# Kernel tuning notes

Measured on AMD Instinct MI355X. Metric: run time of the kernel, lower is better.

Reference implementation:

```python
import jax, jax.numpy as jnp
import numpy as np

MODE_STATIC = 0
MODE_APPEARANCE_CHANGE = 2
MODE_BLINK = 3
MODE_AFFINE = 4


def _affine_warp(src, theta):
    """F.affine_grid + F.grid_sample(bilinear, zeros, align_corners=False).

    src:   [N, C, H, W]
    theta: [N, 2, 3]
    """
    N, C, H, W = src.shape
    dt = src.dtype
    # affine_grid base coords (align_corners=False): centers of pixels in [-1, 1]
    xs = (jnp.arange(W, dtype=dt) * 2 + 1) / W - 1  # [W]
    ys = (jnp.arange(H, dtype=dt) * 2 + 1) / H - 1  # [H]
    gx = (theta[:, 0, 0][:, None, None] * xs[None, None, :]
          + theta[:, 0, 1][:, None, None] * ys[None, :, None]
          + theta[:, 0, 2][:, None, None])  # [N, H, W]
    gy = (theta[:, 1, 0][:, None, None] * xs[None, None, :]
          + theta[:, 1, 1][:, None, None] * ys[None, :, None]
          + theta[:, 1, 2][:, None, None])  # [N, H, W]
    # unnormalize (align_corners=False)
    ix = ((gx + 1) * W - 1) / 2
    iy = ((gy + 1) * H - 1) / 2
    x0 = jnp.floor(ix)
    y0 = jnp.floor(iy)
    wx1 = ix - x0
    wy1 = iy - y0
    wx0 = 1 - wx1
    wy0 = 1 - wy1
    x0i = x0.astype(jnp.int32)
    y0i = y0.astype(jnp.int32)

    src_flat = src.reshape(N, C, H * W)

    def gather(xi, yi):
        valid = (xi >= 0) & (xi < W) & (yi >= 0) & (yi < H)  # zeros padding
        xi_c = jnp.clip(xi, 0, W - 1)
        yi_c = jnp.clip(yi, 0, H - 1)
        idx = (yi_c * W + xi_c).reshape(N, 1, H * W)
        v = jnp.take_along_axis(src_flat, idx, axis=2).reshape(N, C, H, W)
        return v * valid.astype(dt)[:, None]

    out = (gather(x0i, y0i) * (wx0 * wy0)[:, None]
           + gather(x0i + 1, y0i) * (wx1 * wy0)[:, None]
           + gather(x0i, y0i + 1) * (wx0 * wy1)[:, None]
           + gather(x0i + 1, y0i + 1) * (wx1 * wy1)[:, None])
    return out


def setup_inputs() -> dict:
    key = jax.random.key(0)
    ks = jax.random.split(key, 7)
    B, NI, C, H, W = 4, 16, 3, 256, 256
    g0 = jax.random.normal(ks[0], (B, NI, C, H, W), dtype=jnp.float32)
    m0 = jax.random.uniform(ks[1], (B, NI, 1, H, W), dtype=jnp.float32)
    mode_logits = jax.random.normal(ks[2], (B, NI, 5), dtype=jnp.float32)
    # near-identity affine transforms (realistic small motions)
    ident = jnp.array([1.0, 0.0, 0.0, 0.0, 1.0, 0.0], dtype=jnp.float32)
    transform_params = ident + 0.1 * jax.random.normal(ks[3], (B, NI, 6), dtype=jnp.float32)
    alpha = jax.random.uniform(ks[4], (B, NI, 1), dtype=jnp.float32)
    instance_valid = (jax.random.uniform(ks[5], (B, NI)) > 0.2).astype(jnp.float32)
    i_bg = jax.random.normal(ks[6], (B, C, H, W), dtype=jnp.float32)
    return {"g0": g0, "m0": m0, "mode_logits": mode_logits,
            "transform_params": transform_params, "alpha": alpha,
            "instance_valid": instance_valid, "i_bg": i_bg}


def reference(g0, m0, mode_logits, transform_params, alpha, instance_valid, i_bg):
    B, NI, C, H, W = g0.shape
    theta = transform_params.reshape(-1, 2, 3)  # [B*NI, 2, 3]
    warped_overlay = _affine_warp(g0.reshape(B * NI, C, H, W), theta).reshape(B, NI, C, H, W)
    warped_mask = _affine_warp(m0.reshape(B * NI, 1, H, W), theta).reshape(B, NI, 1, H, W)

    mode_ids = jnp.argmax(mode_logits, axis=-1)  # [B, NI]
    static_like = ((mode_ids == MODE_STATIC) | (mode_ids == MODE_APPEARANCE_CHANGE)
                   | (mode_ids == MODE_AFFINE)).astype(g0.dtype)[:, :, None, None, None]
    blink = (mode_ids == MODE_BLINK).astype(g0.dtype)[:, :, None, None, None]
    alpha_map = alpha[:, :, :, None, None]  # [B, NI, 1, 1, 1]
    valid = instance_valid[:, :, None, None, None]

    g_mid_per_instance = (static_like * warped_overlay + blink * warped_overlay * alpha_map) * valid
    m_mid_per_instance = (static_like * warped_mask + blink * warped_mask * alpha_map) * valid
    g_mid = g_mid_per_instance.sum(axis=1)
    m_mid = jnp.clip(m_mid_per_instance.sum(axis=1), 0.0, 1.0)
    i_base = i_bg + g_mid
    return (g_mid_per_instance, m_mid_per_instance, g_mid, m_mid, i_base)
```

## Files before the change

kernel.cpp:

```cpp
#include <hip/hip_runtime.h>

#define BB 4
#define NI 16
#define CC 3
#define HH 256
#define WW 256
#define HWSZ (HH * WW)

__device__ __forceinline__ float inst_params(
    const float* __restrict__ ml, const float* __restrict__ tp,
    const float* __restrict__ al, const float* __restrict__ iv,
    int id, float th[6]) {
    float best = ml[id * 5];
    int bid = 0;
#pragma unroll
    for (int k = 1; k < 5; ++k) {
        float v = ml[id * 5 + k];
        if (v > best) { best = v; bid = k; }
    }
    float coef = (bid == 0 || bid == 2 || bid == 4) ? 1.0f
               : (bid == 3 ? al[id] : 0.0f);
    coef *= iv[id];
#pragma unroll
    for (int k = 0; k < 6; ++k) th[k] = tp[id * 6 + k];
    return coef;
}

struct Samp {
    int o00, o10, o01, o11;
    float w00, w10, w01, w11;
};

__device__ __forceinline__ Samp make_samp(const float th[6], int p) {
    const int h = p >> 8, w = p & (WW - 1);
    const float xs = (2 * w + 1) * (1.0f / WW) - 1.0f;
    const float ys = (2 * h + 1) * (1.0f / HH) - 1.0f;
    const float gx = th[0] * xs + th[1] * ys + th[2];
    const float gy = th[3] * xs + th[4] * ys + th[5];
    const float ix = gx * (0.5f * WW) + (0.5f * WW - 0.5f);
    const float iy = gy * (0.5f * HH) + (0.5f * HH - 0.5f);
    const float x0f = floorf(ix), y0f = floorf(iy);
    const float wx1 = ix - x0f, wy1 = iy - y0f;
    const float wx0 = 1.0f - wx1, wy0 = 1.0f - wy1;
    const int x0 = (int)x0f, y0 = (int)y0f;
    const int x1 = x0 + 1, y1 = y0 + 1;
    const float wx0v = ((unsigned)x0 < (unsigned)WW) ? wx0 : 0.0f;
    const float wx1v = ((unsigned)x1 < (unsigned)WW) ? wx1 : 0.0f;
    const float wy0v = ((unsigned)y0 < (unsigned)HH) ? wy0 : 0.0f;
    const float wy1v = ((unsigned)y1 < (unsigned)HH) ? wy1 : 0.0f;
    const int x0c = min(max(x0, 0), WW - 1), x1c = min(max(x1, 0), WW - 1);
    const int y0c = min(max(y0, 0), HH - 1), y1c = min(max(y1, 0), HH - 1);
    Samp s;
    s.o00 = y0c * WW + x0c; s.o10 = y0c * WW + x1c;
    s.o01 = y1c * WW + x0c; s.o11 = y1c * WW + x1c;
    s.w00 = wx0v * wy0v; s.w10 = wx1v * wy0v;
    s.w01 = wx0v * wy1v; s.w11 = wx1v * wy1v;
    return s;
}

__device__ __forceinline__ float bilerp(const float* __restrict__ src, const Samp& s) {
    return s.w00 * src[s.o00] + s.w10 * src[s.o10]
         + s.w01 * src[s.o01] + s.w11 * src[s.o11];
}

__global__ __launch_bounds__(256) void warp_inst(
    const float* __restrict__ g0,
    const float* __restrict__ m0,
    const float* __restrict__ ml,
    const float* __restrict__ tp,
    const float* __restrict__ al,
    const float* __restrict__ iv,
    float* __restrict__ out_gpi,
    float* __restrict__ out_mpi) {
    const int id = blockIdx.y;
    const int p0 = blockIdx.x * 512 + threadIdx.x;

    float th[6];
    const float coef = inst_params(ml, tp, al, iv, id, th);

    float* gp = out_gpi + (size_t)id * CC * HWSZ + p0;
    float* mp = out_mpi + (size_t)id * HWSZ + p0;

    if (coef == 0.0f) {
        gp[0] = 0.0f;            gp[WW] = 0.0f;
        gp[HWSZ] = 0.0f;         gp[HWSZ + WW] = 0.0f;
        gp[2 * HWSZ] = 0.0f;     gp[2 * HWSZ + WW] = 0.0f;
        mp[0] = 0.0f;            mp[WW] = 0.0f;
        return;
    }

    const Samp sa = make_samp(th, p0);
    const Samp sb = make_samp(th, p0 + WW);

    const float* gsrc = g0 + (size_t)id * CC * HWSZ;
    const float* msrc = m0 + (size_t)id * HWSZ;

    const float v0a = coef * bilerp(gsrc, sa);
    const float v0b = coef * bilerp(gsrc, sb);
    const float v1a = coef * bilerp(gsrc + HWSZ, sa);
    const float v1b = coef * bilerp(gsrc + HWSZ, sb);
    const float v2a = coef * bilerp(gsrc + 2 * HWSZ, sa);
    const float v2b = coef * bilerp(gsrc + 2 * HWSZ, sb);
    const float vma = coef * bilerp(msrc, sa);
    const float vmb = coef * bilerp(msrc, sb);

    gp[0] = v0a;            gp[WW] = v0b;
    gp[HWSZ] = v1a;         gp[HWSZ + WW] = v1b;
    gp[2 * HWSZ] = v2a;     gp[2 * HWSZ + WW] = v2b;
    mp[0] = vma;            mp[WW] = vmb;
}

__global__ __launch_bounds__(128) void combine_k(
    const float* __restrict__ gpi,
    const float* __restrict__ mpi,
    const float* __restrict__ i_bg,
    float* __restrict__ out_gmid,
    float* __restrict__ out_mmid,
    float* __restrict__ out_ibase) {
    const int b = blockIdx.y;
    const int pix = (blockIdx.x * 128 + threadIdx.x) * 4;

    float4 s0 = make_float4(0.f, 0.f, 0.f, 0.f);
    float4 s1 = s0, s2 = s0, sm = s0;
#pragma unroll
    for (int ii = 0; ii < NI; ++ii) {
        const float* gb = gpi + (size_t)(b * NI + ii) * CC * HWSZ + pix;
        const float4 a0 = *(const float4*)(gb);
        const float4 a1 = *(const float4*)(gb + HWSZ);
        const float4 a2 = *(const float4*)(gb + 2 * HWSZ);
        const float4 am = *(const float4*)(mpi + (size_t)(b * NI + ii) * HWSZ + pix);
        s0.x += a0.x; s0.y += a0.y; s0.z += a0.z; s0.w += a0.w;
        s1.x += a1.x; s1.y += a1.y; s1.z += a1.z; s1.w += a1.w;
        s2.x += a2.x; s2.y += a2.y; s2.z += a2.z; s2.w += a2.w;
        sm.x += am.x; sm.y += am.y; sm.z += am.z; sm.w += am.w;
    }
    const size_t ob = (size_t)b * CC * HWSZ + pix;
    const float4 bg0 = *(const float4*)(i_bg + ob);
    const float4 bg1 = *(const float4*)(i_bg + ob + HWSZ);
    const float4 bg2 = *(const float4*)(i_bg + ob + 2 * HWSZ);

    *(float4*)(out_gmid + ob)            = s0;
    *(float4*)(out_gmid + ob + HWSZ)     = s1;
    *(float4*)(out_gmid + ob + 2 * HWSZ) = s2;
    *(float4*)(out_ibase + ob) =
        make_float4(s0.x + bg0.x, s0.y + bg0.y, s0.z + bg0.z, s0.w + bg0.w);
    *(float4*)(out_ibase + ob + HWSZ) =
        make_float4(s1.x + bg1.x, s1.y + bg1.y, s1.z + bg1.z, s1.w + bg1.w);
    *(float4*)(out_ibase + ob + 2 * HWSZ) =
        make_float4(s2.x + bg2.x, s2.y + bg2.y, s2.z + bg2.z, s2.w + bg2.w);
    *(float4*)(out_mmid + (size_t)b * HWSZ + pix) =
        make_float4(fminf(fmaxf(sm.x, 0.f), 1.f), fminf(fmaxf(sm.y, 0.f), 1.f),
                    fminf(fmaxf(sm.z, 0.f), 1.f), fminf(fmaxf(sm.w, 0.f), 1.f));
}

extern "C" void kernel_launch(void* const* d_in, const int* in_sizes, int n_in,
                              void* d_out, int out_size, void* d_ws, size_t ws_size,
                              hipStream_t stream) {
    const float* g0          = (const float*)d_in[0];
    const float* m0          = (const float*)d_in[1];
    const float* mode_logits = (const float*)d_in[2];
    const float* tp          = (const float*)d_in[3];
    const float* alpha       = (const float*)d_in[4];
    const float* iv          = (const float*)d_in[5];
    const float* i_bg        = (const float*)d_in[6];

    float* out       = (float*)d_out;
    float* out_gpi   = out;
    float* out_mpi   = out_gpi  + (size_t)BB * NI * CC * HWSZ;
    float* out_gmid  = out_mpi  + (size_t)BB * NI * HWSZ;
    float* out_mmid  = out_gmid + (size_t)BB * CC * HWSZ;
    float* out_ibase = out_mmid + (size_t)BB * HWSZ;

    dim3 grid1(HWSZ / 512, BB * NI);
    warp_inst<<<grid1, 256, 0, stream>>>(g0, m0, mode_logits, tp, alpha, iv,
                                         out_gpi, out_mpi);

    dim3 grid2(HWSZ / 4 / 128, BB);
    combine_k<<<grid2, 128, 0, stream>>>(out_gpi, out_mpi, i_bg,
                                         out_gmid, out_mmid, out_ibase);
}
```

Baseline: 155.2 us.

## Fuse per-instance warp and instance reduction into a single kernel

Merges the warp kernel and the combine kernel so each thread warps all 16 instances for one pixel, writes per-instance outputs with nontemporal stores, and accumulates the sums in registers. This removes the re-read of the full per-instance intermediate arrays and one kernel launch. In exchange, each thread processes instances serially, which lowers per-thread memory-level parallelism, and the float4 vector accesses become scalar.

```diff
diff --git a/kernel.cpp b/kernel.cpp
--- a/kernel.cpp
+++ b/kernel.cpp
@@ -63,94 +63,58 @@
          + s.w01 * src[s.o01] + s.w11 * src[s.o11];
 }
 
-__global__ __launch_bounds__(256) void warp_inst(
+__global__ __launch_bounds__(512) void fused_k(
     const float* __restrict__ g0,
     const float* __restrict__ m0,
     const float* __restrict__ ml,
     const float* __restrict__ tp,
     const float* __restrict__ al,
     const float* __restrict__ iv,
+    const float* __restrict__ i_bg,
     float* __restrict__ out_gpi,
-    float* __restrict__ out_mpi) {
-    const int id = blockIdx.y;
-    const int p0 = blockIdx.x * 512 + threadIdx.x;
-
-    float th[6];
-    const float coef = inst_params(ml, tp, al, iv, id, th);
-
-    float* gp = out_gpi + (size_t)id * CC * HWSZ + p0;
-    float* mp = out_mpi + (size_t)id * HWSZ + p0;
-
-    if (coef == 0.0f) {
-        gp[0] = 0.0f;            gp[WW] = 0.0f;
-        gp[HWSZ] = 0.0f;         gp[HWSZ + WW] = 0.0f;
-        gp[2 * HWSZ] = 0.0f;     gp[2 * HWSZ + WW] = 0.0f;
-        mp[0] = 0.0f;            mp[WW] = 0.0f;
-        return;
-    }
-
-    const Samp sa = make_samp(th, p0);
-    const Samp sb = make_samp(th, p0 + WW);
-
-    const float* gsrc = g0 + (size_t)id * CC * HWSZ;
-    const float* msrc = m0 + (size_t)id * HWSZ;
-
-    const float v0a = coef * bilerp(gsrc, sa);
-    const float v0b = coef * bilerp(gsrc, sb);
-    const float v1a = coef * bilerp(gsrc + HWSZ, sa);
-    const float v1b = coef * bilerp(gsrc + HWSZ, sb);
-    const float v2a = coef * bilerp(gsrc + 2 * HWSZ, sa);
-    const float v2b = coef * bilerp(gsrc + 2 * HWSZ, sb);
-    const float vma = coef * bilerp(msrc, sa);
-    const float vmb = coef * bilerp(msrc, sb);
-
-    gp[0] = v0a;            gp[WW] = v0b;
-    gp[HWSZ] = v1a;         gp[HWSZ + WW] = v1b;
-    gp[2 * HWSZ] = v2a;     gp[2 * HWSZ + WW] = v2b;
-    mp[0] = vma;            mp[WW] = vmb;
-}
-
-__global__ __launch_bounds__(128) void combine_k(
-    const float* __restrict__ gpi,
-    const float* __restrict__ mpi,
-    const float* __restrict__ i_bg,
+    float* __restrict__ out_mpi,
     float* __restrict__ out_gmid,
     float* __restrict__ out_mmid,
     float* __restrict__ out_ibase) {
     const int b = blockIdx.y;
-    const int pix = (blockIdx.x * 128 + threadIdx.x) * 4;
+    const int p = blockIdx.x * 512 + threadIdx.x;
 
-    float4 s0 = make_float4(0.f, 0.f, 0.f, 0.f);
-    float4 s1 = s0, s2 = s0, sm = s0;
-#pragma unroll
+    float s0 = 0.f, s1 = 0.f, s2 = 0.f, sm = 0.f;
+
+#pragma unroll 2
     for (int ii = 0; ii < NI; ++ii) {
-        const float* gb = gpi + (size_t)(b * NI + ii) * CC * HWSZ + pix;
-        const float4 a0 = *(const float4*)(gb);
-        const float4 a1 = *(const float4*)(gb + HWSZ);
-        const float4 a2 = *(const float4*)(gb + 2 * HWSZ);
-        const float4 am = *(const float4*)(mpi + (size_t)(b * NI + ii) * HWSZ + pix);
-        s0.x += a0.x; s0.y += a0.y; s0.z += a0.z; s0.w += a0.w;
-        s1.x += a1.x; s1.y += a1.y; s1.z += a1.z; s1.w += a1.w;
-        s2.x += a2.x; s2.y += a2.y; s2.z += a2.z; s2.w += a2.w;
-        sm.x += am.x; sm.y += am.y; sm.z += am.z; sm.w += am.w;
+        const int id = b * NI + ii;
+        float th[6];
+        const float coef = inst_params(ml, tp, al, iv, id, th);
+
+        float v0 = 0.f, v1 = 0.f, v2 = 0.f, vm = 0.f;
+        if (coef != 0.0f) {
+            const Samp s = make_samp(th, p);
+            const float* gsrc = g0 + (size_t)id * CC * HWSZ;
+            const float* msrc = m0 + (size_t)id * HWSZ;
+            v0 = coef * bilerp(gsrc, s);
+            v1 = coef * bilerp(gsrc + HWSZ, s);
+            v2 = coef * bilerp(gsrc + 2 * HWSZ, s);
+            vm = coef * bilerp(msrc, s);
+        }
+
+        float* gp = out_gpi + (size_t)id * CC * HWSZ + p;
+        __builtin_nontemporal_store(v0, gp);
+        __builtin_nontemporal_store(v1, gp + HWSZ);
+        __builtin_nontemporal_store(v2, gp + 2 * HWSZ);
+        __builtin_nontemporal_store(vm, out_mpi + (size_t)id * HWSZ + p);
+
+        s0 += v0; s1 += v1; s2 += v2; sm += vm;
     }
-    const size_t ob = (size_t)b * CC * HWSZ + pix;
-    const float4 bg0 = *(const float4*)(i_bg + ob);
-    const float4 bg1 = *(const float4*)(i_bg + ob + HWSZ);
-    const float4 bg2 = *(const float4*)(i_bg + ob + 2 * HWSZ);
 
-    *(float4*)(out_gmid + ob)            = s0;
-    *(float4*)(out_gmid + ob + HWSZ)     = s1;
-    *(float4*)(out_gmid + ob + 2 * HWSZ) = s2;
-    *(float4*)(out_ibase + ob) =
-        make_float4(s0.x + bg0.x, s0.y + bg0.y, s0.z + bg0.z, s0.w + bg0.w);
-    *(float4*)(out_ibase + ob + HWSZ) =
-        make_float4(s1.x + bg1.x, s1.y + bg1.y, s1.z + bg1.z, s1.w + bg1.w);
-    *(float4*)(out_ibase + ob + 2 * HWSZ) =
-        make_float4(s2.x + bg2.x, s2.y + bg2.y, s2.z + bg2.z, s2.w + bg2.w);
-    *(float4*)(out_mmid + (size_t)b * HWSZ + pix) =
-        make_float4(fminf(fmaxf(sm.x, 0.f), 1.f), fminf(fmaxf(sm.y, 0.f), 1.f),
-                    fminf(fmaxf(sm.z, 0.f), 1.f), fminf(fmaxf(sm.w, 0.f), 1.f));
+    const size_t ob = (size_t)b * CC * HWSZ + p;
+    out_gmid[ob]             = s0;
+    out_gmid[ob + HWSZ]      = s1;
+    out_gmid[ob + 2 * HWSZ]  = s2;
+    out_ibase[ob]            = s0 + i_bg[ob];
+    out_ibase[ob + HWSZ]     = s1 + i_bg[ob + HWSZ];
+    out_ibase[ob + 2 * HWSZ] = s2 + i_bg[ob + 2 * HWSZ];
+    out_mmid[(size_t)b * HWSZ + p] = fminf(fmaxf(sm, 0.f), 1.f);
 }
 
 extern "C" void kernel_launch(void* const* d_in, const int* in_sizes, int n_in,
@@ -171,11 +135,8 @@
     float* out_mmid  = out_gmid + (size_t)BB * CC * HWSZ;
     float* out_ibase = out_mmid + (size_t)BB * HWSZ;
 
-    dim3 grid1(HWSZ / 512, BB * NI);
-    warp_inst<<<grid1, 256, 0, stream>>>(g0, m0, mode_logits, tp, alpha, iv,
-                                         out_gpi, out_mpi);
-
-    dim3 grid2(HWSZ / 4 / 128, BB);
-    combine_k<<<grid2, 128, 0, stream>>>(out_gpi, out_mpi, i_bg,
-                                         out_gmid, out_mmid, out_ibase);
+    dim3 grid(HWSZ / 512, BB);
+    fused_k<<<grid, 512, 0, stream>>>(g0, m0, mode_logits, tp, alpha, iv, i_bg,
+                                      out_gpi, out_mpi,
+                                      out_gmid, out_mmid, out_ibase);
 }
```

Result: no change. 157.2 us (+1.3%).
